# Kernel tuning notes

Hardware: AMD Instinct MI355X
Metric: run time of the kernel (lower is better)

The kernel has to match this reference:

```python
import jax, jax.numpy as jnp
import numpy as np

B, H, W, DIM, NH, HD = 2, 64, 160, 256, 8, 32
R0, R1 = 1, 1                      # win_r (x, y)
WX, WY = 2 * R0 + 2, 2 * R1 + 2    # window extents
A = WX * WY                        # attn_num = 16
SCALE = HD ** (-0.5)


def setup_inputs() -> dict:
    key = jax.random.key(0)
    ks = jax.random.split(key, 6)
    x = jax.random.normal(ks[0], (B, H, W, DIM), jnp.float32)
    # float match positions anywhere in the image; clamp in reference() keeps windows in-bounds
    u = jax.random.uniform(ks[1], (B, H * W, 2), jnp.float32)
    max_offset = u * jnp.array([W, H], jnp.float32)
    Wq = jax.random.normal(ks[2], (DIM, NH * HD), jnp.float32) * 0.02
    Wk = jax.random.normal(ks[3], (DIM, NH * HD), jnp.float32) * 0.02
    Wv = jax.random.normal(ks[4], (DIM, NH * HD), jnp.float32) * 0.02
    Wproj = jax.random.normal(ks[5], (NH * HD, DIM), jnp.float32) * 0.02
    return dict(x=x, max_offset=max_offset, Wq=Wq, Wk=Wk, Wv=Wv, Wproj=Wproj)


def reference(x, max_offset, Wq, Wk, Wv, Wproj):
    b, h, w, _ = x.shape
    n = h * w
    xf = x.reshape(b, n, -1)
    q = (xf @ Wq).reshape(b, n, NH, HD)
    k = (xf @ Wk).reshape(b, n, NH, HD)
    v = (xf @ Wv).reshape(b, n, NH, HD)

    # clamp_max_offset: keep the (2r+2)^2 window fully inside the image
    ox = jnp.clip(max_offset[..., 0], R0, w - 1 - R0 - 0.001)
    oy = jnp.clip(max_offset[..., 1], R1, h - 1 - R1 - 0.001)
    mx, my = jnp.floor(ox), jnp.floor(oy)
    fx, fy = ox - mx, oy - my  # bilinear fractions

    # window gather indices: rows my-R1..my+R1+1, cols mx-R0..mx+R0+1
    ix = mx.astype(jnp.int32)[..., None] + jnp.arange(-R0, R0 + 2)  # (b,n,WX)
    iy = my.astype(jnp.int32)[..., None] + jnp.arange(-R1, R1 + 2)  # (b,n,WY)
    idx = (iy[:, :, :, None] * w + ix[:, :, None, :]).reshape(b, n, A)  # (b,n,A)

    gather = jax.vmap(lambda t, i: t[i])  # per-batch row gather
    kg = gather(k.reshape(b, n, NH * HD), idx).reshape(b, n, A, NH, HD)
    vg = gather(v.reshape(b, n, NH * HD), idx).reshape(b, n, A, NH, HD)

    attn = jnp.einsum('bnhd,bnahd->bnha', q, kg) * SCALE  # (b,n,NH,A)

    # bilinear weights: edge elements weighted by (1-f)/f, interior by 1
    wx = jnp.concatenate([(1 - fx)[..., None], jnp.ones((b, n, 2 * R0), fx.dtype), fx[..., None]], axis=-1)
    wy = jnp.concatenate([(1 - fy)[..., None], jnp.ones((b, n, 2 * R1), fy.dtype), fy[..., None]], axis=-1)
    bw = (wy[:, :, :, None] * wx[:, :, None, :]).reshape(b, n, 1, A)

    # bilinear-weighted stable softmax
    m = jnp.max(attn, axis=-1, keepdims=True)
    e = jnp.exp(attn - m) * bw
    p = e / jnp.sum(e, axis=-1, keepdims=True)

    out = jnp.einsum('bnha,bnahd->bnhd', p, vg).reshape(b, n, NH * HD)
    out = out @ Wproj
    return out.reshape(b, h, w, -1)
```

## Files before the change

kernel.cpp:

```cpp
#include <hip/hip_runtime.h>
#include <math.h>

#define Bb   2
#define Hh   64
#define Ww   160
#define DIMc 256
#define Nn   (Hh * Ww)
#define SCALEf 0.17677669529663687f

typedef unsigned short u16;
typedef unsigned int   u32;
typedef __bf16 bf16x8 __attribute__((ext_vector_type(8)));
typedef float  f32x4  __attribute__((ext_vector_type(4)));

__device__ __forceinline__ u16 f2bf(float f) {
    u32 u = __float_as_uint(f);
    u += 0x7fffu + ((u >> 16) & 1u);
    return (u16)(u >> 16);
}
__device__ __forceinline__ u32 pack2(float lo, float hi) {
    return (u32)f2bf(lo) | ((u32)f2bf(hi) << 16);
}
__device__ __forceinline__ float bflo(u32 u) { return __uint_as_float(u << 16); }
__device__ __forceinline__ float bfhi(u32 u) { return __uint_as_float(u & 0xffff0000u); }

__global__ __launch_bounds__(256) void prep_w(const float* __restrict__ Wq,
                                              const float* __restrict__ Wk,
                                              const float* __restrict__ Wv,
                                              const float* __restrict__ Wp,
                                              u16* __restrict__ WtAll)
{
    int id = blockIdx.x * 256 + threadIdx.x;
    int wsel = id >> 16;
    int rem  = id & 65535;
    int kk = rem >> 8, nn = rem & 255;
    const float* W = (wsel == 0) ? Wq : (wsel == 1) ? Wk : (wsel == 2) ? Wv : Wp;
    WtAll[(size_t)wsel * 65536 + nn * 256 + kk] = f2bf(W[kk * 256 + nn]);
}

template <bool A_IS_F32, bool BF16OUT>
__device__ __forceinline__ void gemm_core(const void* __restrict__ Avoid,
                                          const u16* __restrict__ Btg,
                                          u16* __restrict__ Cb,
                                          float* __restrict__ Cf)
{
    __shared__ __align__(16) char smem[32768];
    u16* sA = (u16*)smem;
    u16* sB = (u16*)(smem + 8192);

    const int t    = threadIdx.x;
    const int lane = t & 63;
    const int wv   = t >> 6;
    const int wm   = wv & 1;
    const int wn   = wv >> 1;
    const int m0   = blockIdx.y * 128;
    const int n0   = blockIdx.x * 128;

    const int r0  = t >> 2;
    const int kc0 = (t & 3) * 8;

    const int col  = lane & 15;
    const int quad = lane >> 4;

    f32x4 acc[4][4];
#pragma unroll
    for (int i = 0; i < 4; ++i)
#pragma unroll
        for (int j = 0; j < 4; ++j)
            acc[i][j] = (f32x4){0.f, 0.f, 0.f, 0.f};

    const float* Af = (const float*)Avoid;
    const u16*   Ab = (const u16*)Avoid;
    const u16*   Bbase = Btg + (size_t)n0 * 256;

    for (int k0 = 0; k0 < 256; k0 += 32) {
        uint4 a0, a1;
        if (A_IS_F32) {
            const float* ap0 = Af + (size_t)(m0 + r0) * 256 + k0 + kc0;
            const float* ap1 = Af + (size_t)(m0 + 64 + r0) * 256 + k0 + kc0;
            float4 f0 = *(const float4*)ap0, f1 = *(const float4*)(ap0 + 4);
            float4 f2 = *(const float4*)ap1, f3 = *(const float4*)(ap1 + 4);
            a0.x = pack2(f0.x, f0.y); a0.y = pack2(f0.z, f0.w);
            a0.z = pack2(f1.x, f1.y); a0.w = pack2(f1.z, f1.w);
            a1.x = pack2(f2.x, f2.y); a1.y = pack2(f2.z, f2.w);
            a1.z = pack2(f3.x, f3.y); a1.w = pack2(f3.z, f3.w);
        } else {
            a0 = *(const uint4*)(Ab + (size_t)(m0 + r0) * 256 + k0 + kc0);
            a1 = *(const uint4*)(Ab + (size_t)(m0 + 64 + r0) * 256 + k0 + kc0);
        }
        uint4 b0 = *(const uint4*)(Bbase + (size_t)r0 * 256 + k0 + kc0);
        uint4 b1 = *(const uint4*)(Bbase + (size_t)(64 + r0) * 256 + k0 + kc0);
        __syncthreads();
        *(uint4*)(sA + r0 * 32 + kc0)        = a0;
        *(uint4*)(sA + (64 + r0) * 32 + kc0) = a1;
        *(uint4*)(sB + r0 * 32 + kc0)        = b0;
        *(uint4*)(sB + (64 + r0) * 32 + kc0) = b1;
        __syncthreads();

        bf16x8 af[4], bfr[4];
#pragma unroll
        for (int mt = 0; mt < 4; ++mt)
            af[mt] = *(const bf16x8*)(sA + (wm * 64 + mt * 16 + col) * 32 + quad * 8);
#pragma unroll
        for (int nt = 0; nt < 4; ++nt)
            bfr[nt] = *(const bf16x8*)(sB + (wn * 64 + nt * 16 + col) * 32 + quad * 8);

#pragma unroll
        for (int mt = 0; mt < 4; ++mt)
#pragma unroll
            for (int nt = 0; nt < 4; ++nt)
                acc[mt][nt] = __builtin_amdgcn_mfma_f32_16x16x32_bf16(af[mt], bfr[nt], acc[mt][nt], 0, 0, 0);
    }

    __syncthreads();
    if (BF16OUT) {
        u16* sC = (u16*)smem;
#pragma unroll
        for (int mt = 0; mt < 4; ++mt)
#pragma unroll
            for (int nt = 0; nt < 4; ++nt) {
                const int rw = wm * 64 + mt * 16 + quad * 4;
                const int cl = wn * 64 + nt * 16 + col;
#pragma unroll
                for (int rr = 0; rr < 4; ++rr)
                    sC[(rw + rr) * 128 + cl] = f2bf(acc[mt][nt][rr]);
            }
        __syncthreads();
#pragma unroll
        for (int i = 0; i < 8; ++i) {
            int j   = i * 256 + t;
            int row = j >> 4;
            int off = (j & 15) * 8;
            *(uint4*)(Cb + (size_t)(m0 + row) * 256 + n0 + off) = *(const uint4*)(sC + row * 128 + off);
        }
    } else {
        float* sC = (float*)smem;
#pragma unroll
        for (int ph = 0; ph < 2; ++ph) {
            if (wm == ph) {
#pragma unroll
                for (int mt = 0; mt < 4; ++mt)
#pragma unroll
                    for (int nt = 0; nt < 4; ++nt) {
                        const int rw = mt * 16 + quad * 4;
                        const int cl = wn * 64 + nt * 16 + col;
#pragma unroll
                        for (int rr = 0; rr < 4; ++rr)
                            sC[(rw + rr) * 128 + cl] = acc[mt][nt][rr];
                    }
            }
            __syncthreads();
#pragma unroll
            for (int i = 0; i < 8; ++i) {
                int j   = i * 256 + t;
                int row = j >> 5;
                int off = (j & 31) * 4;
                *(float4*)(Cf + (size_t)(m0 + ph * 64 + row) * 256 + n0 + off) =
                    *(const float4*)(sC + row * 128 + off);
            }
            __syncthreads();
        }
    }
}

__global__ __launch_bounds__(256) void gemm_qkv(const float* __restrict__ x,
                                                const u16* __restrict__ WtAll,
                                                u16* __restrict__ q,
                                                u16* __restrict__ k,
                                                u16* __restrict__ v)
{
    const int z = blockIdx.z;
    u16* C = (z == 0) ? q : (z == 1) ? k : v;
    gemm_core<true, true>(x, WtAll + (size_t)z * 65536, C, nullptr);
}

__global__ __launch_bounds__(256) void gemm_proj(const u16* __restrict__ ao,
                                                 const u16* __restrict__ WtAll,
                                                 float* __restrict__ out)
{
    gemm_core<false, false>(ao, WtAll + (size_t)3 * 65536, nullptr, out);
}

__global__ __launch_bounds__(256) void attn_kernel(const u16* __restrict__ q,
                                                   const u16* __restrict__ k,
                                                   const u16* __restrict__ v,
                                                   const float* __restrict__ moff,
                                                   u16* __restrict__ ao)
{
    const int wv   = threadIdx.x >> 6;
    const int lane = threadIdx.x & 63;
    const int pos  = blockIdx.x * 4 + wv;
    const int rowbase = (pos >= Nn) ? Nn : 0;

    float2 mo = *(const float2*)(moff + (size_t)pos * 2);
    float ox = fminf(fmaxf(mo.x, 1.0f), (float)(Ww - 2) - 0.001f);
    float oy = fminf(fmaxf(mo.y, 1.0f), (float)(Hh - 2) - 0.001f);
    float mxf = floorf(ox), myf = floorf(oy);
    float fx = ox - mxf, fy = oy - myf;
    int imx = (int)mxf, imy = (int)myf;

    const int h  = lane & 7;
    const int a0 = lane >> 3;

    uint4 q4[4];
    {
        const uint4* qp = (const uint4*)(q + (size_t)pos * 256 + h * 32);
#pragma unroll
        for (int jj = 0; jj < 4; ++jj) q4[jj] = qp[jj];
    }

    float s[2];
#pragma unroll
    for (int p = 0; p < 2; ++p) {
        int a   = a0 + 8 * p;
        int row = rowbase + (imy + (a >> 2) - 1) * Ww + imx + (a & 3) - 1;
        const uint4* kp = (const uint4*)(k + (size_t)row * 256 + h * 32);
        float acc = 0.f;
#pragma unroll
        for (int jj = 0; jj < 4; ++jj) {
            uint4 kw = kp[jj];
            acc += bflo(q4[jj].x) * bflo(kw.x) + bfhi(q4[jj].x) * bfhi(kw.x)
                 + bflo(q4[jj].y) * bflo(kw.y) + bfhi(q4[jj].y) * bfhi(kw.y)
                 + bflo(q4[jj].z) * bflo(kw.z) + bfhi(q4[jj].z) * bfhi(kw.z)
                 + bflo(q4[jj].w) * bflo(kw.w) + bfhi(q4[jj].w) * bfhi(kw.w);
        }
        s[p] = acc * SCALEf;
    }

    auto wc = [](int r, float f) { return r == 0 ? 1.f - f : (r == 3 ? f : 1.f); };
    float bw0 = wc(a0 >> 2, fy) * wc(a0 & 3, fx);
    float bw1 = wc((a0 + 8) >> 2, fy) * wc(a0 & 3, fx);

    float m = fmaxf(s[0], s[1]);
    m = fmaxf(m, __shfl_xor(m, 8));
    m = fmaxf(m, __shfl_xor(m, 16));
    m = fmaxf(m, __shfl_xor(m, 32));
    float e0 = expf(s[0] - m) * bw0;
    float e1 = expf(s[1] - m) * bw1;
    float sum = e0 + e1;
    sum += __shfl_xor(sum, 8);
    sum += __shfl_xor(sum, 16);
    sum += __shfl_xor(sum, 32);
    float inv = 1.f / sum;
    float p0 = e0 * inv, p1 = e1 * inv;

    float acc0 = 0.f, acc1 = 0.f, acc2 = 0.f, acc3 = 0.f;
    const int myh = lane >> 3;
#pragma unroll
    for (int a = 0; a < 16; ++a) {
        int row = rowbase + (imy + (a >> 2) - 1) * Ww + imx + (a & 3) - 1;
        uint2 vw = *(const uint2*)(v + (size_t)row * 256 + 4 * lane);
        int src = ((a & 7) << 3) | myh;
        float pa = __shfl(a < 8 ? p0 : p1, src);
        acc0 += pa * bflo(vw.x); acc1 += pa * bfhi(vw.x);
        acc2 += pa * bflo(vw.y); acc3 += pa * bfhi(vw.y);
    }
    uint2 o;
    o.x = pack2(acc0, acc1);
    o.y = pack2(acc2, acc3);
    *(uint2*)(ao + (size_t)pos * 256 + 4 * lane) = o;
}

extern "C" void kernel_launch(void* const* d_in, const int* in_sizes, int n_in,
                              void* d_out, int out_size, void* d_ws, size_t ws_size,
                              hipStream_t stream)
{
    const float* x     = (const float*)d_in[0];
    const float* moff  = (const float*)d_in[1];
    const float* Wq    = (const float*)d_in[2];
    const float* Wk    = (const float*)d_in[3];
    const float* Wv    = (const float*)d_in[4];
    const float* Wproj = (const float*)d_in[5];
    float* out = (float*)d_out;

    const size_t NTOT = (size_t)Bb * Nn * DIMc;
    u16* ws    = (u16*)d_ws;
    u16* WtAll = ws;
    u16* q     = WtAll + 4 * 65536;
    u16* k     = q + NTOT;
    u16* v     = k + NTOT;
    u16* ao    = v + NTOT;

    prep_w<<<dim3(1024), dim3(256), 0, stream>>>(Wq, Wk, Wv, Wproj, WtAll);
    gemm_qkv<<<dim3(2, 160, 3), dim3(256), 0, stream>>>(x, WtAll, q, k, v);
    attn_kernel<<<dim3(Bb * Nn / 4), dim3(256), 0, stream>>>(q, k, v, moff, ao);
    gemm_proj<<<dim3(2, 160, 1), dim3(256), 0, stream>>>(ao, WtAll, out);
}
```

Baseline: 144.7 us.

## Pre-convert x to bf16 and load GEMM tiles via direct global-to-LDS loads

Adds a prep pass that converts x to bf16 once, alongside the weight transpose, instead of converting it inside every QKV GEMM tile. Each of the 6 column-block/z combinations re-read the f32 x before, so this removes redundant conversion and halves A-tile read bytes. GEMM tile staging now uses global_load_lds so data goes straight into LDS without a register round trip. The cost is an extra bf16 buffer write and read of x. The LDS layout per wave has to match the old r0/kc0 indexing, which assumes the 16-byte-per-lane contiguous layout.

```diff
diff --git a/kernel.cpp b/kernel.cpp
--- a/kernel.cpp
+++ b/kernel.cpp
@@ -24,22 +24,43 @@
 __device__ __forceinline__ float bflo(u32 u) { return __uint_as_float(u << 16); }
 __device__ __forceinline__ float bfhi(u32 u) { return __uint_as_float(u & 0xffff0000u); }
 
-__global__ __launch_bounds__(256) void prep_w(const float* __restrict__ Wq,
-                                              const float* __restrict__ Wk,
-                                              const float* __restrict__ Wv,
-                                              const float* __restrict__ Wp,
-                                              u16* __restrict__ WtAll)
-{
-    int id = blockIdx.x * 256 + threadIdx.x;
-    int wsel = id >> 16;
-    int rem  = id & 65535;
-    int kk = rem >> 8, nn = rem & 255;
-    const float* W = (wsel == 0) ? Wq : (wsel == 1) ? Wk : (wsel == 2) ? Wv : Wp;
-    WtAll[(size_t)wsel * 65536 + nn * 256 + kk] = f2bf(W[kk * 256 + nn]);
-}
-
-template <bool A_IS_F32, bool BF16OUT>
-__device__ __forceinline__ void gemm_core(const void* __restrict__ Avoid,
+__device__ __forceinline__ void gload16(const void* g, void* l) {
+    __builtin_amdgcn_global_load_lds(
+        (const __attribute__((address_space(1))) unsigned int*)g,
+        (__attribute__((address_space(3))) unsigned int*)l,
+        16, 0, 0);
+}
+
+#define XCVT_BLOCKS 2560
+__global__ __launch_bounds__(256) void prep(const float* __restrict__ x,
+                                            const float* __restrict__ Wq,
+                                            const float* __restrict__ Wk,
+                                            const float* __restrict__ Wv,
+                                            const float* __restrict__ Wp,
+                                            u16* __restrict__ WtAll,
+                                            u16* __restrict__ xb)
+{
+    const int b = blockIdx.x;
+    if (b < XCVT_BLOCKS) {
+        const int id = b * 256 + threadIdx.x;
+        const float4* xp = (const float4*)x + (size_t)id * 2;
+        float4 f0 = xp[0], f1 = xp[1];
+        uint4 o;
+        o.x = pack2(f0.x, f0.y); o.y = pack2(f0.z, f0.w);
+        o.z = pack2(f1.x, f1.y); o.w = pack2(f1.z, f1.w);
+        *(uint4*)(xb + (size_t)id * 8) = o;
+    } else {
+        const int id = (b - XCVT_BLOCKS) * 256 + threadIdx.x;
+        const int wsel = id >> 16;
+        const int rem  = id & 65535;
+        const int kk = rem >> 8, nn = rem & 255;
+        const float* W = (wsel == 0) ? Wq : (wsel == 1) ? Wk : (wsel == 2) ? Wv : Wp;
+        WtAll[(size_t)wsel * 65536 + nn * 256 + kk] = f2bf(W[kk * 256 + nn]);
+    }
+}
+
+template <bool BF16OUT>
+__device__ __forceinline__ void gemm_core(const u16* __restrict__ Ab,
                                           const u16* __restrict__ Btg,
                                           u16* __restrict__ Cb,
                                           float* __restrict__ Cf)
@@ -69,32 +90,18 @@
         for (int j = 0; j < 4; ++j)
             acc[i][j] = (f32x4){0.f, 0.f, 0.f, 0.f};
 
-    const float* Af = (const float*)Avoid;
-    const u16*   Ab = (const u16*)Avoid;
-    const u16*   Bbase = Btg + (size_t)n0 * 256;
+    const u16* Bbase = Btg + (size_t)n0 * 256;
+    char* ldsA0 = smem + wv * 1024;
+    char* ldsA1 = smem + 4096 + wv * 1024;
+    char* ldsB0 = smem + 8192 + wv * 1024;
+    char* ldsB1 = smem + 8192 + 4096 + wv * 1024;
 
     for (int k0 = 0; k0 < 256; k0 += 32) {
-        uint4 a0, a1;
-        if (A_IS_F32) {
-            const float* ap0 = Af + (size_t)(m0 + r0) * 256 + k0 + kc0;
-            const float* ap1 = Af + (size_t)(m0 + 64 + r0) * 256 + k0 + kc0;
-            float4 f0 = *(const float4*)ap0, f1 = *(const float4*)(ap0 + 4);
-            float4 f2 = *(const float4*)ap1, f3 = *(const float4*)(ap1 + 4);
-            a0.x = pack2(f0.x, f0.y); a0.y = pack2(f0.z, f0.w);
-            a0.z = pack2(f1.x, f1.y); a0.w = pack2(f1.z, f1.w);
-            a1.x = pack2(f2.x, f2.y); a1.y = pack2(f2.z, f2.w);
-            a1.z = pack2(f3.x, f3.y); a1.w = pack2(f3.z, f3.w);
-        } else {
-            a0 = *(const uint4*)(Ab + (size_t)(m0 + r0) * 256 + k0 + kc0);
-            a1 = *(const uint4*)(Ab + (size_t)(m0 + 64 + r0) * 256 + k0 + kc0);
-        }
-        uint4 b0 = *(const uint4*)(Bbase + (size_t)r0 * 256 + k0 + kc0);
-        uint4 b1 = *(const uint4*)(Bbase + (size_t)(64 + r0) * 256 + k0 + kc0);
         __syncthreads();
-        *(uint4*)(sA + r0 * 32 + kc0)        = a0;
-        *(uint4*)(sA + (64 + r0) * 32 + kc0) = a1;
-        *(uint4*)(sB + r0 * 32 + kc0)        = b0;
-        *(uint4*)(sB + (64 + r0) * 32 + kc0) = b1;
+        gload16(Ab    + (size_t)(m0 + r0)      * 256 + k0 + kc0, ldsA0);
+        gload16(Ab    + (size_t)(m0 + 64 + r0) * 256 + k0 + kc0, ldsA1);
+        gload16(Bbase + (size_t)r0             * 256 + k0 + kc0, ldsB0);
+        gload16(Bbase + (size_t)(64 + r0)      * 256 + k0 + kc0, ldsB1);
         __syncthreads();
 
         bf16x8 af[4], bfr[4];
@@ -163,7 +170,7 @@
     }
 }
 
-__global__ __launch_bounds__(256) void gemm_qkv(const float* __restrict__ x,
+__global__ __launch_bounds__(256) void gemm_qkv(const u16* __restrict__ xb,
                                                 const u16* __restrict__ WtAll,
                                                 u16* __restrict__ q,
                                                 u16* __restrict__ k,
@@ -171,14 +178,14 @@
 {
     const int z = blockIdx.z;
     u16* C = (z == 0) ? q : (z == 1) ? k : v;
-    gemm_core<true, true>(x, WtAll + (size_t)z * 65536, C, nullptr);
+    gemm_core<true>(xb, WtAll + (size_t)z * 65536, C, nullptr);
 }
 
 __global__ __launch_bounds__(256) void gemm_proj(const u16* __restrict__ ao,
                                                  const u16* __restrict__ WtAll,
                                                  float* __restrict__ out)
 {
-    gemm_core<false, false>(ao, WtAll + (size_t)3 * 65536, nullptr, out);
+    gemm_core<false>(ao, WtAll + (size_t)3 * 65536, nullptr, out);
 }
 
 __global__ __launch_bounds__(256) void attn_kernel(const u16* __restrict__ q,
@@ -280,9 +287,10 @@
     u16* k     = q + NTOT;
     u16* v     = k + NTOT;
     u16* ao    = v + NTOT;
-
-    prep_w<<<dim3(1024), dim3(256), 0, stream>>>(Wq, Wk, Wv, Wproj, WtAll);
-    gemm_qkv<<<dim3(2, 160, 3), dim3(256), 0, stream>>>(x, WtAll, q, k, v);
+    u16* xb    = ao + NTOT;
+
+    prep<<<dim3(XCVT_BLOCKS + 1024), dim3(256), 0, stream>>>(x, Wq, Wk, Wv, Wproj, WtAll, xb);
+    gemm_qkv<<<dim3(2, 160, 3), dim3(256), 0, stream>>>(xb, WtAll, q, k, v);
     attn_kernel<<<dim3(Bb * Nn / 4), dim3(256), 0, stream>>>(q, k, v, moff, ao);
     gemm_proj<<<dim3(2, 160, 1), dim3(256), 0, stream>>>(ao, WtAll, out);
 }
```

After: 145.5 us. About the same (+0.5%).

## Fuse windowed attention with output projection and load QKV weights via LDS DMA

Applied to the files above, without the earlier changes.

The attention kernel now computes 16 positions per block, stores the bf16 attention output in swizzled shared memory, and immediately runs the output projection with MFMA. This removes the separate projection GEMM and the global round trip of the attention output. The QKV GEMM also loads weight tiles straight into LDS with global_load_lds, bypassing registers. In exchange, each 16-row block reads the full projection weight tile straight from global memory without LDS reuse, and the MFMA tile is smaller.

```diff
diff --git a/kernel.cpp b/kernel.cpp
--- a/kernel.cpp
+++ b/kernel.cpp
@@ -24,6 +24,13 @@
 __device__ __forceinline__ float bflo(u32 u) { return __uint_as_float(u << 16); }
 __device__ __forceinline__ float bfhi(u32 u) { return __uint_as_float(u & 0xffff0000u); }
 
+__device__ __forceinline__ void gload16(const void* g, void* l) {
+    __builtin_amdgcn_global_load_lds(
+        (const __attribute__((address_space(1))) unsigned int*)g,
+        (__attribute__((address_space(3))) unsigned int*)l,
+        16, 0, 0);
+}
+
 __global__ __launch_bounds__(256) void prep_w(const float* __restrict__ Wq,
                                               const float* __restrict__ Wk,
                                               const float* __restrict__ Wv,
@@ -38,15 +45,19 @@
     WtAll[(size_t)wsel * 65536 + nn * 256 + kk] = f2bf(W[kk * 256 + nn]);
 }
 
-template <bool A_IS_F32, bool BF16OUT>
-__device__ __forceinline__ void gemm_core(const void* __restrict__ Avoid,
-                                          const u16* __restrict__ Btg,
-                                          u16* __restrict__ Cb,
-                                          float* __restrict__ Cf)
+__global__ __launch_bounds__(256) void gemm_qkv(const float* __restrict__ x,
+                                                const u16* __restrict__ WtAll,
+                                                u16* __restrict__ q,
+                                                u16* __restrict__ k,
+                                                u16* __restrict__ v)
 {
     __shared__ __align__(16) char smem[32768];
     u16* sA = (u16*)smem;
     u16* sB = (u16*)(smem + 8192);
+
+    const int z = blockIdx.z;
+    u16* Cb = (z == 0) ? q : (z == 1) ? k : v;
+    const u16* Btg = WtAll + (size_t)z * 65536;
 
     const int t    = threadIdx.x;
     const int lane = t & 63;
@@ -69,32 +80,26 @@
         for (int j = 0; j < 4; ++j)
             acc[i][j] = (f32x4){0.f, 0.f, 0.f, 0.f};
 
-    const float* Af = (const float*)Avoid;
-    const u16*   Ab = (const u16*)Avoid;
-    const u16*   Bbase = Btg + (size_t)n0 * 256;
+    const u16* Bbase = Btg + (size_t)n0 * 256;
+    char* ldsB0 = smem + 8192 + wv * 1024;
+    char* ldsB1 = smem + 8192 + 4096 + wv * 1024;
 
     for (int k0 = 0; k0 < 256; k0 += 32) {
+        const float* ap0 = x + (size_t)(m0 + r0) * 256 + k0 + kc0;
+        const float* ap1 = x + (size_t)(m0 + 64 + r0) * 256 + k0 + kc0;
+        float4 f0 = *(const float4*)ap0, f1 = *(const float4*)(ap0 + 4);
+        float4 f2 = *(const float4*)ap1, f3 = *(const float4*)(ap1 + 4);
         uint4 a0, a1;
-        if (A_IS_F32) {
-            const float* ap0 = Af + (size_t)(m0 + r0) * 256 + k0 + kc0;
-            const float* ap1 = Af + (size_t)(m0 + 64 + r0) * 256 + k0 + kc0;
-            float4 f0 = *(const float4*)ap0, f1 = *(const float4*)(ap0 + 4);
-            float4 f2 = *(const float4*)ap1, f3 = *(const float4*)(ap1 + 4);
-            a0.x = pack2(f0.x, f0.y); a0.y = pack2(f0.z, f0.w);
-            a0.z = pack2(f1.x, f1.y); a0.w = pack2(f1.z, f1.w);
-            a1.x = pack2(f2.x, f2.y); a1.y = pack2(f2.z, f2.w);
-            a1.z = pack2(f3.x, f3.y); a1.w = pack2(f3.z, f3.w);
-        } else {
-            a0 = *(const uint4*)(Ab + (size_t)(m0 + r0) * 256 + k0 + kc0);
-            a1 = *(const uint4*)(Ab + (size_t)(m0 + 64 + r0) * 256 + k0 + kc0);
-        }
-        uint4 b0 = *(const uint4*)(Bbase + (size_t)r0 * 256 + k0 + kc0);
-        uint4 b1 = *(const uint4*)(Bbase + (size_t)(64 + r0) * 256 + k0 + kc0);
+        a0.x = pack2(f0.x, f0.y); a0.y = pack2(f0.z, f0.w);
+        a0.z = pack2(f1.x, f1.y); a0.w = pack2(f1.z, f1.w);
+        a1.x = pack2(f2.x, f2.y); a1.y = pack2(f2.z, f2.w);
+        a1.z = pack2(f3.x, f3.y); a1.w = pack2(f3.z, f3.w);
+
         __syncthreads();
         *(uint4*)(sA + r0 * 32 + kc0)        = a0;
         *(uint4*)(sA + (64 + r0) * 32 + kc0) = a1;
-        *(uint4*)(sB + r0 * 32 + kc0)        = b0;
-        *(uint4*)(sB + (64 + r0) * 32 + kc0) = b1;
+        gload16(Bbase + (size_t)r0        * 256 + k0 + kc0, ldsB0);
+        gload16(Bbase + (size_t)(64 + r0) * 256 + k0 + kc0, ldsB1);
         __syncthreads();
 
         bf16x8 af[4], bfr[4];
@@ -113,152 +118,141 @@
     }
 
     __syncthreads();
-    if (BF16OUT) {
-        u16* sC = (u16*)smem;
-#pragma unroll
-        for (int mt = 0; mt < 4; ++mt)
-#pragma unroll
-            for (int nt = 0; nt < 4; ++nt) {
-                const int rw = wm * 64 + mt * 16 + quad * 4;
-                const int cl = wn * 64 + nt * 16 + col;
-#pragma unroll
-                for (int rr = 0; rr < 4; ++rr)
-                    sC[(rw + rr) * 128 + cl] = f2bf(acc[mt][nt][rr]);
-            }
-        __syncthreads();
-#pragma unroll
-        for (int i = 0; i < 8; ++i) {
-            int j   = i * 256 + t;
-            int row = j >> 4;
-            int off = (j & 15) * 8;
-            *(uint4*)(Cb + (size_t)(m0 + row) * 256 + n0 + off) = *(const uint4*)(sC + row * 128 + off);
-        }
-    } else {
-        float* sC = (float*)smem;
-#pragma unroll
-        for (int ph = 0; ph < 2; ++ph) {
-            if (wm == ph) {
-#pragma unroll
-                for (int mt = 0; mt < 4; ++mt)
-#pragma unroll
-                    for (int nt = 0; nt < 4; ++nt) {
-                        const int rw = mt * 16 + quad * 4;
-                        const int cl = wn * 64 + nt * 16 + col;
-#pragma unroll
-                        for (int rr = 0; rr < 4; ++rr)
-                            sC[(rw + rr) * 128 + cl] = acc[mt][nt][rr];
-                    }
-            }
-            __syncthreads();
-#pragma unroll
-            for (int i = 0; i < 8; ++i) {
-                int j   = i * 256 + t;
-                int row = j >> 5;
-                int off = (j & 31) * 4;
-                *(float4*)(Cf + (size_t)(m0 + ph * 64 + row) * 256 + n0 + off) =
-                    *(const float4*)(sC + row * 128 + off);
-            }
-            __syncthreads();
-        }
-    }
-}
-
-__global__ __launch_bounds__(256) void gemm_qkv(const float* __restrict__ x,
-                                                const u16* __restrict__ WtAll,
-                                                u16* __restrict__ q,
-                                                u16* __restrict__ k,
-                                                u16* __restrict__ v)
-{
-    const int z = blockIdx.z;
-    u16* C = (z == 0) ? q : (z == 1) ? k : v;
-    gemm_core<true, true>(x, WtAll + (size_t)z * 65536, C, nullptr);
-}
-
-__global__ __launch_bounds__(256) void gemm_proj(const u16* __restrict__ ao,
-                                                 const u16* __restrict__ WtAll,
+    u16* sC = (u16*)smem;
+#pragma unroll
+    for (int mt = 0; mt < 4; ++mt)
+#pragma unroll
+        for (int nt = 0; nt < 4; ++nt) {
+            const int rw = wm * 64 + mt * 16 + quad * 4;
+            const int cl = wn * 64 + nt * 16 + col;
+#pragma unroll
+            for (int rr = 0; rr < 4; ++rr)
+                sC[(rw + rr) * 128 + cl] = f2bf(acc[mt][nt][rr]);
+        }
+    __syncthreads();
+#pragma unroll
+    for (int i = 0; i < 8; ++i) {
+        int j   = i * 256 + t;
+        int row = j >> 4;
+        int off = (j & 15) * 8;
+        *(uint4*)(Cb + (size_t)(m0 + row) * 256 + n0 + off) = *(const uint4*)(sC + row * 128 + off);
+    }
+}
+
+__global__ __launch_bounds__(256) void attn_proj(const u16* __restrict__ q,
+                                                 const u16* __restrict__ k,
+                                                 const u16* __restrict__ v,
+                                                 const float* __restrict__ moff,
+                                                 const u16* __restrict__ Wpt,
                                                  float* __restrict__ out)
 {
-    gemm_core<false, false>(ao, WtAll + (size_t)3 * 65536, nullptr, out);
-}
-
-__global__ __launch_bounds__(256) void attn_kernel(const u16* __restrict__ q,
-                                                   const u16* __restrict__ k,
-                                                   const u16* __restrict__ v,
-                                                   const float* __restrict__ moff,
-                                                   u16* __restrict__ ao)
-{
+    __shared__ __align__(16) u16 aoS[16 * 256];
+
     const int wv   = threadIdx.x >> 6;
     const int lane = threadIdx.x & 63;
-    const int pos  = blockIdx.x * 4 + wv;
-    const int rowbase = (pos >= Nn) ? Nn : 0;
-
-    float2 mo = *(const float2*)(moff + (size_t)pos * 2);
-    float ox = fminf(fmaxf(mo.x, 1.0f), (float)(Ww - 2) - 0.001f);
-    float oy = fminf(fmaxf(mo.y, 1.0f), (float)(Hh - 2) - 0.001f);
-    float mxf = floorf(ox), myf = floorf(oy);
-    float fx = ox - mxf, fy = oy - myf;
-    int imx = (int)mxf, imy = (int)myf;
-
-    const int h  = lane & 7;
-    const int a0 = lane >> 3;
-
-    uint4 q4[4];
-    {
-        const uint4* qp = (const uint4*)(q + (size_t)pos * 256 + h * 32);
-#pragma unroll
-        for (int jj = 0; jj < 4; ++jj) q4[jj] = qp[jj];
-    }
-
-    float s[2];
-#pragma unroll
-    for (int p = 0; p < 2; ++p) {
-        int a   = a0 + 8 * p;
-        int row = rowbase + (imy + (a >> 2) - 1) * Ww + imx + (a & 3) - 1;
-        const uint4* kp = (const uint4*)(k + (size_t)row * 256 + h * 32);
-        float acc = 0.f;
-#pragma unroll
-        for (int jj = 0; jj < 4; ++jj) {
-            uint4 kw = kp[jj];
-            acc += bflo(q4[jj].x) * bflo(kw.x) + bfhi(q4[jj].x) * bfhi(kw.x)
-                 + bflo(q4[jj].y) * bflo(kw.y) + bfhi(q4[jj].y) * bfhi(kw.y)
-                 + bflo(q4[jj].z) * bflo(kw.z) + bfhi(q4[jj].z) * bfhi(kw.z)
-                 + bflo(q4[jj].w) * bflo(kw.w) + bfhi(q4[jj].w) * bfhi(kw.w);
-        }
-        s[p] = acc * SCALEf;
-    }
-
-    auto wc = [](int r, float f) { return r == 0 ? 1.f - f : (r == 3 ? f : 1.f); };
-    float bw0 = wc(a0 >> 2, fy) * wc(a0 & 3, fx);
-    float bw1 = wc((a0 + 8) >> 2, fy) * wc(a0 & 3, fx);
-
-    float m = fmaxf(s[0], s[1]);
-    m = fmaxf(m, __shfl_xor(m, 8));
-    m = fmaxf(m, __shfl_xor(m, 16));
-    m = fmaxf(m, __shfl_xor(m, 32));
-    float e0 = expf(s[0] - m) * bw0;
-    float e1 = expf(s[1] - m) * bw1;
-    float sum = e0 + e1;
-    sum += __shfl_xor(sum, 8);
-    sum += __shfl_xor(sum, 16);
-    sum += __shfl_xor(sum, 32);
-    float inv = 1.f / sum;
-    float p0 = e0 * inv, p1 = e1 * inv;
-
-    float acc0 = 0.f, acc1 = 0.f, acc2 = 0.f, acc3 = 0.f;
-    const int myh = lane >> 3;
-#pragma unroll
-    for (int a = 0; a < 16; ++a) {
-        int row = rowbase + (imy + (a >> 2) - 1) * Ww + imx + (a & 3) - 1;
-        uint2 vw = *(const uint2*)(v + (size_t)row * 256 + 4 * lane);
-        int src = ((a & 7) << 3) | myh;
-        float pa = __shfl(a < 8 ? p0 : p1, src);
-        acc0 += pa * bflo(vw.x); acc1 += pa * bfhi(vw.x);
-        acc2 += pa * bflo(vw.y); acc3 += pa * bfhi(vw.y);
-    }
-    uint2 o;
-    o.x = pack2(acc0, acc1);
-    o.y = pack2(acc2, acc3);
-    *(uint2*)(ao + (size_t)pos * 256 + 4 * lane) = o;
+    const int quad = lane >> 4;
+    const int h    = lane & 7;
+    const int a0   = lane >> 3;
+    const int myh  = lane >> 3;
+
+    for (int i = 0; i < 4; ++i) {
+        const int m   = wv * 4 + i;
+        const int pos = blockIdx.x * 16 + m;
+        const int rowbase = (pos >= Nn) ? Nn : 0;
+
+        float2 mo = *(const float2*)(moff + (size_t)pos * 2);
+        float ox = fminf(fmaxf(mo.x, 1.0f), (float)(Ww - 2) - 0.001f);
+        float oy = fminf(fmaxf(mo.y, 1.0f), (float)(Hh - 2) - 0.001f);
+        float mxf = floorf(ox), myf = floorf(oy);
+        float fx = ox - mxf, fy = oy - myf;
+        int imx = (int)mxf, imy = (int)myf;
+
+        uint4 q4[4];
+        {
+            const uint4* qp = (const uint4*)(q + (size_t)pos * 256 + h * 32);
+#pragma unroll
+            for (int jj = 0; jj < 4; ++jj) q4[jj] = qp[jj];
+        }
+
+        float s[2];
+#pragma unroll
+        for (int p = 0; p < 2; ++p) {
+            int a   = a0 + 8 * p;
+            int row = rowbase + (imy + (a >> 2) - 1) * Ww + imx + (a & 3) - 1;
+            const uint4* kp = (const uint4*)(k + (size_t)row * 256 + h * 32);
+            float acc = 0.f;
+#pragma unroll
+            for (int jj = 0; jj < 4; ++jj) {
+                uint4 kw = kp[jj];
+                acc += bflo(q4[jj].x) * bflo(kw.x) + bfhi(q4[jj].x) * bfhi(kw.x)
+                     + bflo(q4[jj].y) * bflo(kw.y) + bfhi(q4[jj].y) * bfhi(kw.y)
+                     + bflo(q4[jj].z) * bflo(kw.z) + bfhi(q4[jj].z) * bfhi(kw.z)
+                     + bflo(q4[jj].w) * bflo(kw.w) + bfhi(q4[jj].w) * bfhi(kw.w);
+            }
+            s[p] = acc * SCALEf;
+        }
+
+        auto wc = [](int r, float f) { return r == 0 ? 1.f - f : (r == 3 ? f : 1.f); };
+        float bw0 = wc(a0 >> 2, fy) * wc(a0 & 3, fx);
+        float bw1 = wc((a0 + 8) >> 2, fy) * wc(a0 & 3, fx);
+
+        float mx = fmaxf(s[0], s[1]);
+        mx = fmaxf(mx, __shfl_xor(mx, 8));
+        mx = fmaxf(mx, __shfl_xor(mx, 16));
+        mx = fmaxf(mx, __shfl_xor(mx, 32));
+        float e0 = expf(s[0] - mx) * bw0;
+        float e1 = expf(s[1] - mx) * bw1;
+        float sum = e0 + e1;
+        sum += __shfl_xor(sum, 8);
+        sum += __shfl_xor(sum, 16);
+        sum += __shfl_xor(sum, 32);
+        float inv = 1.f / sum;
+        float p0 = e0 * inv, p1 = e1 * inv;
+
+        float acc0 = 0.f, acc1 = 0.f, acc2 = 0.f, acc3 = 0.f;
+#pragma unroll
+        for (int a = 0; a < 16; ++a) {
+            int row = rowbase + (imy + (a >> 2) - 1) * Ww + imx + (a & 3) - 1;
+            uint2 vw = *(const uint2*)(v + (size_t)row * 256 + 4 * lane);
+            int src = ((a & 7) << 3) | myh;
+            float pa = __shfl(a < 8 ? p0 : p1, src);
+            acc0 += pa * bflo(vw.x); acc1 += pa * bfhi(vw.x);
+            acc2 += pa * bflo(vw.y); acc3 += pa * bfhi(vw.y);
+        }
+        uint2 o;
+        o.x = pack2(acc0, acc1);
+        o.y = pack2(acc2, acc3);
+        u32 off = (u32)m * 512 + (((u32)lane * 8) ^ (u32)((m & 7) << 4));
+        *(uint2*)((char*)aoS + off) = o;
+    }
+
+    __syncthreads();
+
+    f32x4 pacc[4];
+#pragma unroll
+    for (int nt = 0; nt < 4; ++nt) pacc[nt] = (f32x4){0.f, 0.f, 0.f, 0.f};
+
+    const int mrow = lane & 15;
+#pragma unroll
+    for (int k0 = 0; k0 < 256; k0 += 32) {
+        u32 aoff = (u32)mrow * 512 + (((u32)((k0 + quad * 8) * 2)) ^ (u32)((mrow & 7) << 4));
+        bf16x8 afr = *(const bf16x8*)((const char*)aoS + aoff);
+#pragma unroll
+        for (int nt = 0; nt < 4; ++nt) {
+            const u16* bp = Wpt + (size_t)(wv * 64 + nt * 16 + mrow) * 256 + k0 + quad * 8;
+            bf16x8 bfr = *(const bf16x8*)bp;
+            pacc[nt] = __builtin_amdgcn_mfma_f32_16x16x32_bf16(afr, bfr, pacc[nt], 0, 0, 0);
+        }
+    }
+
+    const int m0 = blockIdx.x * 16;
+#pragma unroll
+    for (int nt = 0; nt < 4; ++nt) {
+        const int cl = wv * 64 + nt * 16 + mrow;
+#pragma unroll
+        for (int rr = 0; rr < 4; ++rr)
+            out[(size_t)(m0 + quad * 4 + rr) * 256 + cl] = pacc[nt][rr];
+    }
 }
 
 extern "C" void kernel_launch(void* const* d_in, const int* in_sizes, int n_in,
@@ -279,10 +273,9 @@
     u16* q     = WtAll + 4 * 65536;
     u16* k     = q + NTOT;
     u16* v     = k + NTOT;
-    u16* ao    = v + NTOT;
 
     prep_w<<<dim3(1024), dim3(256), 0, stream>>>(Wq, Wk, Wv, Wproj, WtAll);
     gemm_qkv<<<dim3(2, 160, 3), dim3(256), 0, stream>>>(x, WtAll, q, k, v);
-    attn_kernel<<<dim3(Bb * Nn / 4), dim3(256), 0, stream>>>(q, k, v, moff, ao);
-    gemm_proj<<<dim3(2, 160, 1), dim3(256), 0, stream>>>(ao, WtAll, out);
-}
+    attn_proj<<<dim3(Bb * Nn / 16), dim3(256), 0, stream>>>(q, k, v, moff,
+                                                            WtAll + (size_t)3 * 65536, out);
+}
```

New measurement: 178.8 us. 1.24x slower.

## Counting-sort query positions by window key and use direct-to-LDS loads in GEMMs

Applied to the files above, without the earlier changes.

Adds a counting sort (count, single-block scan, scatter) that groups query positions by their clamped window origin. The attention kernel then processes positions in sorted order, with an XCD-aware block remap, so neighbouring waves gather overlapping K/V rows and get better L2 reuse. Separately, the GEMMs now stage their bf16 operands with global_load_lds instead of going through registers. The cost is three extra small launches, one of them a serial single-block scan, plus atomics, and attention output writes become scattered.

```diff
diff --git a/kernel.cpp b/kernel.cpp
--- a/kernel.cpp
+++ b/kernel.cpp
@@ -6,6 +6,7 @@
 #define Ww   160
 #define DIMc 256
 #define Nn   (Hh * Ww)
+#define NPOS (Bb * Nn)
 #define SCALEf 0.17677669529663687f
 
 typedef unsigned short u16;
@@ -24,29 +25,93 @@
 __device__ __forceinline__ float bflo(u32 u) { return __uint_as_float(u << 16); }
 __device__ __forceinline__ float bfhi(u32 u) { return __uint_as_float(u & 0xffff0000u); }
 
+__device__ __forceinline__ void gload16(const void* g, void* l) {
+    __builtin_amdgcn_global_load_lds(
+        (const __attribute__((address_space(1))) unsigned int*)g,
+        (__attribute__((address_space(3))) unsigned int*)l,
+        16, 0, 0);
+}
+
+__device__ __forceinline__ int win_key(const float* moff, int pos) {
+    float2 mo = *(const float2*)(moff + (size_t)pos * 2);
+    float ox = fminf(fmaxf(mo.x, 1.0f), (float)(Ww - 2) - 0.001f);
+    float oy = fminf(fmaxf(mo.y, 1.0f), (float)(Hh - 2) - 0.001f);
+    int imx = (int)floorf(ox), imy = (int)floorf(oy);
+    return ((pos >= Nn) ? Nn : 0) + imy * Ww + imx;
+}
+
 __global__ __launch_bounds__(256) void prep_w(const float* __restrict__ Wq,
                                               const float* __restrict__ Wk,
                                               const float* __restrict__ Wv,
                                               const float* __restrict__ Wp,
-                                              u16* __restrict__ WtAll)
+                                              u16* __restrict__ WtAll,
+                                              u32* __restrict__ hist)
 {
     int id = blockIdx.x * 256 + threadIdx.x;
-    int wsel = id >> 16;
-    int rem  = id & 65535;
-    int kk = rem >> 8, nn = rem & 255;
-    const float* W = (wsel == 0) ? Wq : (wsel == 1) ? Wk : (wsel == 2) ? Wv : Wp;
-    WtAll[(size_t)wsel * 65536 + nn * 256 + kk] = f2bf(W[kk * 256 + nn]);
-}
-
-template <bool A_IS_F32, bool BF16OUT>
-__device__ __forceinline__ void gemm_core(const void* __restrict__ Avoid,
-                                          const u16* __restrict__ Btg,
-                                          u16* __restrict__ Cb,
-                                          float* __restrict__ Cf)
+    if (id < 262144) {
+        int wsel = id >> 16;
+        int rem  = id & 65535;
+        int kk = rem >> 8, nn = rem & 255;
+        const float* W = (wsel == 0) ? Wq : (wsel == 1) ? Wk : (wsel == 2) ? Wv : Wp;
+        WtAll[(size_t)wsel * 65536 + nn * 256 + kk] = f2bf(W[kk * 256 + nn]);
+    } else {
+        hist[id - 262144] = 0u;
+    }
+}
+
+__global__ __launch_bounds__(256) void sort_count(const float* __restrict__ moff,
+                                                  u32* __restrict__ keys,
+                                                  u32* __restrict__ hist)
+{
+    int pos = blockIdx.x * 256 + threadIdx.x;
+    int key = win_key(moff, pos);
+    keys[pos] = (u32)key;
+    atomicAdd(&hist[key], 1u);
+}
+
+__global__ __launch_bounds__(1024) void sort_scan(u32* __restrict__ hist)
+{
+    __shared__ u32 sc[1024];
+    const int t = threadIdx.x;
+    u32 loc[20];
+    u32 s = 0;
+#pragma unroll
+    for (int j = 0; j < 20; ++j) { loc[j] = hist[t * 20 + j]; s += loc[j]; }
+    sc[t] = s;
+    __syncthreads();
+    for (int off = 1; off < 1024; off <<= 1) {
+        u32 vv = (t >= off) ? sc[t - off] : 0u;
+        __syncthreads();
+        sc[t] += vv;
+        __syncthreads();
+    }
+    u32 ex = sc[t] - s;
+#pragma unroll
+    for (int j = 0; j < 20; ++j) { hist[t * 20 + j] = ex; ex += loc[j]; }
+}
+
+__global__ __launch_bounds__(256) void sort_scatter(const u32* __restrict__ keys,
+                                                    u32* __restrict__ hist,
+                                                    u32* __restrict__ perm)
+{
+    int pos = blockIdx.x * 256 + threadIdx.x;
+    u32 idx = atomicAdd(&hist[keys[pos]], 1u);
+    perm[idx] = (u32)pos;
+}
+
+__global__ __launch_bounds__(256) void gemm_qkv(const float* __restrict__ x,
+                                                const u16* __restrict__ WtAll,
+                                                u16* __restrict__ q,
+                                                u16* __restrict__ k,
+                                                u16* __restrict__ v)
 {
     __shared__ __align__(16) char smem[32768];
     u16* sA = (u16*)smem;
     u16* sB = (u16*)(smem + 8192);
+
+    const int z = blockIdx.z;
+    u16* Cb = (z == 0) ? q : (z == 1) ? k : v;
+    const u16* Btg = WtAll + (size_t)z * 65536;
 
     const int t    = threadIdx.x;
     const int lane = t & 63;
@@ -69,32 +134,26 @@
         for (int j = 0; j < 4; ++j)
             acc[i][j] = (f32x4){0.f, 0.f, 0.f, 0.f};
 
-    const float* Af = (const float*)Avoid;
-    const u16*   Ab = (const u16*)Avoid;
-    const u16*   Bbase = Btg + (size_t)n0 * 256;
+    const u16* Bbase = Btg + (size_t)n0 * 256;
+    char* ldsB0 = smem + 8192 + wv * 1024;
+    char* ldsB1 = smem + 8192 + 4096 + wv * 1024;
 
     for (int k0 = 0; k0 < 256; k0 += 32) {
+        const float* ap0 = x + (size_t)(m0 + r0) * 256 + k0 + kc0;
+        const float* ap1 = x + (size_t)(m0 + 64 + r0) * 256 + k0 + kc0;
+        float4 f0 = *(const float4*)ap0, f1 = *(const float4*)(ap0 + 4);
+        float4 f2 = *(const float4*)ap1, f3 = *(const float4*)(ap1 + 4);
         uint4 a0, a1;
-        if (A_IS_F32) {
-            const float* ap0 = Af + (size_t)(m0 + r0) * 256 + k0 + kc0;
-            const float* ap1 = Af + (size_t)(m0 + 64 + r0) * 256 + k0 + kc0;
-            float4 f0 = *(const float4*)ap0, f1 = *(const float4*)(ap0 + 4);
-            float4 f2 = *(const float4*)ap1, f3 = *(const float4*)(ap1 + 4);
-            a0.x = pack2(f0.x, f0.y); a0.y = pack2(f0.z, f0.w);
-            a0.z = pack2(f1.x, f1.y); a0.w = pack2(f1.z, f1.w);
-            a1.x = pack2(f2.x, f2.y); a1.y = pack2(f2.z, f2.w);
-            a1.z = pack2(f3.x, f3.y); a1.w = pack2(f3.z, f3.w);
-        } else {
-            a0 = *(const uint4*)(Ab + (size_t)(m0 + r0) * 256 + k0 + kc0);
-            a1 = *(const uint4*)(Ab + (size_t)(m0 + 64 + r0) * 256 + k0 + kc0);
-        }
-        uint4 b0 = *(const uint4*)(Bbase + (size_t)r0 * 256 + k0 + kc0);
-        uint4 b1 = *(const uint4*)(Bbase + (size_t)(64 + r0) * 256 + k0 + kc0);
+        a0.x = pack2(f0.x, f0.y); a0.y = pack2(f0.z, f0.w);
+        a0.z = pack2(f1.x, f1.y); a0.w = pack2(f1.z, f1.w);
+        a1.x = pack2(f2.x, f2.y); a1.y = pack2(f2.z, f2.w);
+        a1.z = pack2(f3.x, f3.y); a1.w = pack2(f3.z, f3.w);
+
         __syncthreads();
         *(uint4*)(sA + r0 * 32 + kc0)        = a0;
         *(uint4*)(sA + (64 + r0) * 32 + kc0) = a1;
-        *(uint4*)(sB + r0 * 32 + kc0)        = b0;
-        *(uint4*)(sB + (64 + r0) * 32 + kc0) = b1;
+        gload16(Bbase + (size_t)r0        * 256 + k0 + kc0, ldsB0);
+        gload16(Bbase + (size_t)(64 + r0) * 256 + k0 + kc0, ldsB1);
         __syncthreads();
 
         bf16x8 af[4], bfr[4];
@@ -113,83 +172,39 @@
     }
 
     __syncthreads();
-    if (BF16OUT) {
-        u16* sC = (u16*)smem;
-#pragma unroll
-        for (int mt = 0; mt < 4; ++mt)
-#pragma unroll
-            for (int nt = 0; nt < 4; ++nt) {
-                const int rw = wm * 64 + mt * 16 + quad * 4;
-                const int cl = wn * 64 + nt * 16 + col;
-#pragma unroll
-                for (int rr = 0; rr < 4; ++rr)
-                    sC[(rw + rr) * 128 + cl] = f2bf(acc[mt][nt][rr]);
-            }
-        __syncthreads();
-#pragma unroll
-        for (int i = 0; i < 8; ++i) {
-            int j   = i * 256 + t;
-            int row = j >> 4;
-            int off = (j & 15) * 8;
-            *(uint4*)(Cb + (size_t)(m0 + row) * 256 + n0 + off) = *(const uint4*)(sC + row * 128 + off);
+    u16* sC = (u16*)smem;
+#pragma unroll
+    for (int mt = 0; mt < 4; ++mt)
+#pragma unroll
+        for (int nt = 0; nt < 4; ++nt) {
+            const int rw = wm * 64 + mt * 16 + quad * 4;
+            const int cl = wn * 64 + nt * 16 + col;
+#pragma unroll
+            for (int rr = 0; rr < 4; ++rr)
+                sC[(rw + rr) * 128 + cl] = f2bf(acc[mt][nt][rr]);
         }
-    } else {
-        float* sC = (float*)smem;
-#pragma unroll
-        for (int ph = 0; ph < 2; ++ph) {
-            if (wm == ph) {
-#pragma unroll
-                for (int mt = 0; mt < 4; ++mt)
-#pragma unroll
-                    for (int nt = 0; nt < 4; ++nt) {
-                        const int rw = mt * 16 + quad * 4;
-                        const int cl = wn * 64 + nt * 16 + col;
-#pragma unroll
-                        for (int rr = 0; rr < 4; ++rr)
-                            sC[(rw + rr) * 128 + cl] = acc[mt][nt][rr];
-                    }
-            }
-            __syncthreads();
-#pragma unroll
-            for (int i = 0; i < 8; ++i) {
-                int j   = i * 256 + t;
-                int row = j >> 5;
-                int off = (j & 31) * 4;
-                *(float4*)(Cf + (size_t)(m0 + ph * 64 + row) * 256 + n0 + off) =
-                    *(const float4*)(sC + row * 128 + off);
-            }
-            __syncthreads();
-        }
-    }
-}
-
-__global__ __launch_bounds__(256) void gemm_qkv(const float* __restrict__ x,
-                                                const u16* __restrict__ WtAll,
-                                                u16* __restrict__ q,
-                                                u16* __restrict__ k,
-                                                u16* __restrict__ v)
-{
-    const int z = blockIdx.z;
-    u16* C = (z == 0) ? q : (z == 1) ? k : v;
-    gemm_core<true, true>(x, WtAll + (size_t)z * 65536, C, nullptr);
-}
-
-__global__ __launch_bounds__(256) void gemm_proj(const u16* __restrict__ ao,
-                                                 const u16* __restrict__ WtAll,
-                                                 float* __restrict__ out)
-{
-    gemm_core<false, false>(ao, WtAll + (size_t)3 * 65536, nullptr, out);
+    __syncthreads();
+#pragma unroll
+    for (int i = 0; i < 8; ++i) {
+        int j   = i * 256 + t;
+        int row = j >> 4;
+        int off = (j & 15) * 8;
+        *(uint4*)(Cb + (size_t)(m0 + row) * 256 + n0 + off) = *(const uint4*)(sC + row * 128 + off);
+    }
 }
 
 __global__ __launch_bounds__(256) void attn_kernel(const u16* __restrict__ q,
                                                    const u16* __restrict__ k,
                                                    const u16* __restrict__ v,
                                                    const float* __restrict__ moff,
+                                                   const u32* __restrict__ perm,
                                                    u16* __restrict__ ao)
 {
     const int wv   = threadIdx.x >> 6;
     const int lane = threadIdx.x & 63;
-    const int pos  = blockIdx.x * 4 + wv;
+    const int bid  = blockIdx.x;
+    const int wg   = (bid & 7) * 640 + (bid >> 3);
+    const int pos  = (int)perm[wg * 4 + wv];
     const int rowbase = (pos >= Nn) ? Nn : 0;
 
     float2 mo = *(const float2*)(moff + (size_t)pos * 2);
@@ -261,6 +276,93 @@
     *(uint2*)(ao + (size_t)pos * 256 + 4 * lane) = o;
 }
 
+__global__ __launch_bounds__(256) void gemm_proj(const u16* __restrict__ Ab,
+                                                 const u16* __restrict__ Btg,
+                                                 float* __restrict__ Cf)
+{
+    __shared__ __align__(16) char smem[32768];
+    u16* sA = (u16*)smem;
+    u16* sB = (u16*)(smem + 8192);
+
+    const int t    = threadIdx.x;
+    const int lane = t & 63;
+    const int wv   = t >> 6;
+    const int wm   = wv & 1;
+    const int wn   = wv >> 1;
+    const int m0   = blockIdx.y * 128;
+    const int n0   = blockIdx.x * 128;
+
+    const int r0  = t >> 2;
+    const int kc0 = (t & 3) * 8;
+
+    const int col  = lane & 15;
+    const int quad = lane >> 4;
+
+    f32x4 acc[4][4];
+#pragma unroll
+    for (int i = 0; i < 4; ++i)
+#pragma unroll
+        for (int j = 0; j < 4; ++j)
+            acc[i][j] = (f32x4){0.f, 0.f, 0.f, 0.f};
+
+    const u16* Bbase = Btg + (size_t)n0 * 256;
+    char* ldsA0 = smem + wv * 1024;
+    char* ldsA1 = smem + 4096 + wv * 1024;
+    char* ldsB0 = smem + 8192 + wv * 1024;
+    char* ldsB1 = smem + 8192 + 4096 + wv * 1024;
+
+    for (int k0 = 0; k0 < 256; k0 += 32) {
+        __syncthreads();
+        gload16(Ab    + (size_t)(m0 + r0)      * 256 + k0 + kc0, ldsA0);
+        gload16(Ab    + (size_t)(m0 + 64 + r0) * 256 + k0 + kc0, ldsA1);
+        gload16(Bbase + (size_t)r0             * 256 + k0 + kc0, ldsB0);
+        gload16(Bbase + (size_t)(64 + r0)      * 256 + k0 + kc0, ldsB1);
+        __syncthreads();
+
+        bf16x8 af[4], bfr[4];
+#pragma unroll
+        for (int mt = 0; mt < 4; ++mt)
+            af[mt] = *(const bf16x8*)(sA + (wm * 64 + mt * 16 + col) * 32 + quad * 8);
+#pragma unroll
+        for (int nt = 0; nt < 4; ++nt)
+            bfr[nt] = *(const bf16x8*)(sB + (wn * 64 + nt * 16 + col) * 32 + quad * 8);
+
+#pragma unroll
+        for (int mt = 0; mt < 4; ++mt)
+#pragma unroll
+            for (int nt = 0; nt < 4; ++nt)
+                acc[mt][nt] = __builtin_amdgcn_mfma_f32_16x16x32_bf16(af[mt], bfr[nt], acc[mt][nt], 0, 0, 0);
+    }
+
+    __syncthreads();
+    float* sC = (float*)smem;
+#pragma unroll
+    for (int ph = 0; ph < 2; ++ph) {
+        if (wm == ph) {
+#pragma unroll
+            for (int mt = 0; mt < 4; ++mt)
+#pragma unroll
+                for (int nt = 0; nt < 4; ++nt) {
+                    const int rw = mt * 16 + quad * 4;
+                    const int cl = wn * 64 + nt * 16 + col;
+#pragma unroll
+                    for (int rr = 0; rr < 4; ++rr)
+                        sC[(rw + rr) * 128 + cl] = acc[mt][nt][rr];
+                }
+        }
+        __syncthreads();
+#pragma unroll
+        for (int i = 0; i < 8; ++i) {
+            int j   = i * 256 + t;
+            int row = j >> 5;
+            int off = (j & 31) * 4;
+            *(float4*)(Cf + (size_t)(m0 + ph * 64 + row) * 256 + n0 + off) =
+                *(const float4*)(sC + row * 128 + off);
+        }
+        __syncthreads();
+    }
+}
+
 extern "C" void kernel_launch(void* const* d_in, const int* in_sizes, int n_in,
                               void* d_out, int out_size, void* d_ws, size_t ws_size,
                               hipStream_t stream)
@@ -280,9 +382,15 @@
     u16* k     = q + NTOT;
     u16* v     = k + NTOT;
     u16* ao    = v + NTOT;
-
-    prep_w<<<dim3(1024), dim3(256), 0, stream>>>(Wq, Wk, Wv, Wproj, WtAll);
+    u32* keys  = (u32*)(ao + NTOT);
+    u32* hist  = keys + NPOS;
+    u32* perm  = hist + NPOS;
+
+    prep_w<<<dim3(1104), dim3(256), 0, stream>>>(Wq, Wk, Wv, Wproj, WtAll, hist);
+    sort_count<<<dim3(80), dim3(256), 0, stream>>>(moff, keys, hist);
+    sort_scan<<<dim3(1), dim3(1024), 0, stream>>>(hist);
+    sort_scatter<<<dim3(80), dim3(256), 0, stream>>>(keys, hist, perm);
     gemm_qkv<<<dim3(2, 160, 3), dim3(256), 0, stream>>>(x, WtAll, q, k, v);
-    attn_kernel<<<dim3(Bb * Nn / 4), dim3(256), 0, stream>>>(q, k, v, moff, ao);
-    gemm_proj<<<dim3(2, 160, 1), dim3(256), 0, stream>>>(ao, WtAll, out);
-}
+    attn_kernel<<<dim3(NPOS / 4), dim3(256), 0, stream>>>(q, k, v, moff, perm, ao);
+    gemm_proj<<<dim3(2, 160, 1), dim3(256), 0, stream>>>(ao, WtAll + (size_t)3 * 65536, out);
+}
```

Result: slower. 153.3 us (+5.9%).
